# Optimization experiments

Measured on AMD Instinct MI355X. Metric: run time of the kernel, lower is better.

The kernel has to match this reference:

```python
import jax, jax.numpy as jnp
import numpy as np

DECAY = 0.8
COMMITMENT = 1.0
EPS = 1e-05


def setup_inputs() -> dict:
    key = jax.random.key(0)
    k1, k2 = jax.random.split(key)
    x = jax.random.normal(k1, (8, 4096, 256), dtype=jnp.float32)
    embed = jax.random.normal(k2, (8192, 256), dtype=jnp.float32)
    cluster_size = jnp.zeros((8192,), dtype=jnp.float32)
    embed_avg = embed  # torch registers embed_avg = embed.clone()
    return {"x": x, "embed": embed, "cluster_size": cluster_size, "embed_avg": embed_avg}


def reference(x, embed, cluster_size, embed_avg):
    # EuclideanCodebook.forward (training mode) + VectorQuantize straight-through.
    K, D = embed.shape
    shape = x.shape
    flatten = x.reshape(-1, D)  # [T, D], T = B*N

    dist = (2.0 * (flatten @ embed.T)
            - jnp.sum(flatten * flatten, axis=-1, keepdims=True)
            - jnp.sum(embed * embed, axis=-1)[None, :])  # [T, K]
    embed_ind = jnp.argmax(dist, axis=-1)  # [T]

    quantize = embed[embed_ind].reshape(shape)  # gather

    # EMA codebook statistics (scatter-add instead of materializing one-hot [T,K])
    bins = jax.ops.segment_sum(jnp.ones_like(embed_ind, dtype=x.dtype), embed_ind, num_segments=K)  # [K]
    embed_sum = jax.ops.segment_sum(flatten, embed_ind, num_segments=K)  # [K, D]

    new_cluster_size = cluster_size * DECAY + (1.0 - DECAY) * bins
    new_embed_avg = embed_avg * DECAY + (1.0 - DECAY) * embed_sum

    total = new_cluster_size.sum()
    smoothed = (new_cluster_size + EPS) / (total + K * EPS) * total  # laplace smoothing
    new_embed = new_embed_avg / smoothed[:, None]

    commit_loss = jnp.mean((jax.lax.stop_gradient(quantize) - x) ** 2) * COMMITMENT
    quantize_st = x + jax.lax.stop_gradient(quantize - x)  # straight-through

    ind_out = embed_ind.reshape(shape[:-1])
    return quantize_st, ind_out, commit_loss, new_embed, new_cluster_size, new_embed_avg
```

## Files before the change

kernel.cpp:

```cpp
#include <hip/hip_runtime.h>

#define DECAYF 0.8f
#define OMDF   0.2f
#define EPSF   1e-5f
#define COMMITF 1.0f
#define MARGINF 0.024f
#define FIXCAP  8192
#define MAXR    64

typedef _Float16 h8v __attribute__((ext_vector_type(8)));
typedef float f4v __attribute__((ext_vector_type(4)));

__device__ inline void gload_lds16(const void* g, void* l) {
  __builtin_amdgcn_global_load_lds(
      (const __attribute__((address_space(1))) unsigned int*)g,
      (__attribute__((address_space(3))) unsigned int*)l, 16, 0, 0);
}

__global__ __launch_bounds__(256) void k_pre(
    const float* __restrict__ embed, char* __restrict__ Ews,
    float* __restrict__ zero_p, int zero_n, float* __restrict__ ee, int K, int D)
{
  const int tid = threadIdx.x;
  const int gid0 = blockIdx.x * 256 + tid;
  const int gstride = gridDim.x * 256;

  for (int i = gid0; i < zero_n; i += gstride) zero_p[i] = 0.0f;

  for (int gid = gid0; gid < K * (D / 8); gid += gstride) {
    int k = gid >> 5;
    int d0 = (gid & 31) * 8;
    const float* ep = embed + (size_t)k * D + d0;
    float4 v0 = *(const float4*)(ep);
    float4 v1 = *(const float4*)(ep + 4);
    float f[8] = {v0.x, v0.y, v0.z, v0.w, v1.x, v1.y, v1.z, v1.w};
    h8v h;
    float ss = 0.f;
#pragma unroll
    for (int e = 0; e < 8; ++e) {
      h[e] = (_Float16)f[e];
      ss = fmaf(f[e], f[e], ss);
    }
    int tt = k >> 6;
    int c = k & 63;
    int byteoff = c * 512 + ((d0 * 2) ^ ((c & 7) << 4));
    *(h8v*)(Ews + (size_t)tt * 32768 + byteoff) = h;
#pragma unroll
    for (int off = 1; off < 32; off <<= 1) ss += __shfl_xor(ss, off);
    if ((gid & 31) == 0) ee[k] = 0.5f * ss;
  }
}

__device__ __forceinline__ void upd2(float s, int code, float& b1, float& b2, int& bi) {
  if (s > b1) { b2 = b1; b1 = s; bi = code; }
  else if (s > b2) { b2 = s; }
}

__device__ __forceinline__ void k_body(
    int TT, int NT, char* lds, const char* Ews, const float* ee,
    int w, int lane, int ch, int l15, int rowbyte0,
    const int (&dbyte)[8],
    const h8v (&xh)[2][8],
    f4v (&CUR)[2][2], f4v (&PRV)[2][2],
    float EEP0, float EEP1, float& EEC0, float& EEC1,
    float (&best)[2][4], float (&bst2)[2][4], int (&bidx)[2][4])
{
  const int k0 = TT * 64;
  const char* cb = lds + (TT & 1) * 32768;
  if (TT + 1 < NT) {
    const char* src = Ews + (size_t)(TT + 1) * 32768 + w * 8192 + lane * 16;
    char* dst = lds + ((TT + 1) & 1) * 32768 + w * 8192;
#pragma unroll
    for (int q = 0; q < 8; ++q) gload_lds16(src + q * 1024, dst + q * 1024);
  }
  EEC0 = ee[k0 + ch * 32 + l15];
  EEC1 = ee[k0 + ch * 32 + l15 + 16];
  const int c0p = k0 - 64 + ch * 32 + l15;
  const int c1p = c0p + 16;
#pragma unroll
  for (int rf = 0; rf < 2; ++rf) {
    CUR[rf][0] = (f4v){0.f, 0.f, 0.f, 0.f};
    CUR[rf][1] = (f4v){0.f, 0.f, 0.f, 0.f};
  }
  h8v Bh0[2], Bh1[2];
  {
    const char* p = cb + rowbyte0 + dbyte[0];
    Bh0[0] = *(const h8v*)(p);
    Bh1[0] = *(const h8v*)(p + 8192);
  }
#pragma unroll
  for (int ks = 0; ks < 8; ++ks) {
    const int cs = ks & 1, ns = cs ^ 1;
    if (ks < 7) {
      const char* p = cb + rowbyte0 + dbyte[ks + 1];
      Bh0[ns] = *(const h8v*)(p);
      Bh1[ns] = *(const h8v*)(p + 8192);
    }
    __builtin_amdgcn_s_setprio(1);
    CUR[0][0] = __builtin_amdgcn_mfma_f32_16x16x32_f16(xh[0][ks], Bh0[cs], CUR[0][0], 0, 0, 0);
    CUR[0][1] = __builtin_amdgcn_mfma_f32_16x16x32_f16(xh[0][ks], Bh1[cs], CUR[0][1], 0, 0, 0);
    CUR[1][0] = __builtin_amdgcn_mfma_f32_16x16x32_f16(xh[1][ks], Bh0[cs], CUR[1][0], 0, 0, 0);
    CUR[1][1] = __builtin_amdgcn_mfma_f32_16x16x32_f16(xh[1][ks], Bh1[cs], CUR[1][1], 0, 0, 0);
    __builtin_amdgcn_s_setprio(0);
    {
      const int rf = ks >> 2, ii = ks & 3;
      upd2(PRV[rf][0][ii] - EEP0, c0p, best[rf][ii], bst2[rf][ii], bidx[rf][ii]);
      upd2(PRV[rf][1][ii] - EEP1, c1p, best[rf][ii], bst2[rf][ii], bidx[rf][ii]);
    }
  }
  __syncthreads();
}

__global__ __launch_bounds__(256, 2) void k_dist(
    const float* __restrict__ x, const char* __restrict__ Ews,
    const float* __restrict__ ee, float* __restrict__ ind_f,
    int* __restrict__ idx_out, int* __restrict__ wl, int* __restrict__ cnt,
    int* __restrict__ cntr, int* __restrict__ rlist,
    int* __restrict__ olist, int* __restrict__ ocnt,
    int T, int K)
{
  extern __shared__ char lds[];
  const int tid = threadIdx.x;
  const int w = tid >> 6, lane = tid & 63;
  const int l15 = lane & 15, lk = lane >> 4;
  const int rgrp = w >> 1, ch = w & 1;
  const int row0 = blockIdx.x * 64 + rgrp * 32;
  const int NT = K / 64;

  h8v xh[2][8];
#pragma unroll
  for (int rf = 0; rf < 2; ++rf) {
    const float* xp = x + (size_t)(row0 + rf * 16 + l15) * 256 + lk * 8;
#pragma unroll
    for (int ks = 0; ks < 8; ++ks) {
      float4 v0 = *(const float4*)(xp + ks * 32);
      float4 v1 = *(const float4*)(xp + ks * 32 + 4);
      float f[8] = {v0.x, v0.y, v0.z, v0.w, v1.x, v1.y, v1.z, v1.w};
      h8v h;
#pragma unroll
      for (int e = 0; e < 8; ++e) h[e] = (_Float16)f[e];
      xh[rf][ks] = h;
    }
  }

  float best[2][4], bst2[2][4];
  int bidx[2][4];
#pragma unroll
  for (int rf = 0; rf < 2; ++rf)
#pragma unroll
    for (int i = 0; i < 4; ++i) { best[rf][i] = -3.0e38f; bst2[rf][i] = -3.0e38f; bidx[rf][i] = 0; }

  const int swz = (l15 & 7) << 4;
  const int rowbyte0 = (ch * 32 + l15) * 512;
  int dbyte[8];
#pragma unroll
  for (int ks = 0; ks < 8; ++ks) dbyte[ks] = (ks * 64 + lk * 16) ^ swz;

  {
    const char* src = Ews + (size_t)w * 8192 + lane * 16;
    char* dst = lds + w * 8192;
#pragma unroll
    for (int q = 0; q < 8; ++q)
      gload_lds16(src + q * 1024, dst + q * 1024);
  }
  __syncthreads();

  f4v accA[2][2], accB[2][2];
#pragma unroll
  for (int rf = 0; rf < 2; ++rf) {
    accB[rf][0] = (f4v){-3.0e38f, -3.0e38f, -3.0e38f, -3.0e38f};
    accB[rf][1] = (f4v){-3.0e38f, -3.0e38f, -3.0e38f, -3.0e38f};
  }
  float eeX0 = 0.f, eeX1 = 0.f, eeY0 = 0.f, eeY1 = 0.f;

  for (int tt = 0; tt < NT; tt += 2) {
    k_body(tt,     NT, lds, Ews, ee, w, lane, ch, l15, rowbyte0, dbyte, xh,
           accA, accB, eeX0, eeX1, eeY0, eeY1, best, bst2, bidx);
    k_body(tt + 1, NT, lds, Ews, ee, w, lane, ch, l15, rowbyte0, dbyte, xh,
           accB, accA, eeY0, eeY1, eeX0, eeX1, best, bst2, bidx);
  }
  {
    const int c0 = (NT - 1) * 64 + ch * 32 + l15, c1 = c0 + 16;
#pragma unroll
    for (int rf = 0; rf < 2; ++rf)
#pragma unroll
      for (int ii = 0; ii < 4; ++ii) {
        upd2(accB[rf][0][ii] - eeX0, c0, best[rf][ii], bst2[rf][ii], bidx[rf][ii]);
        upd2(accB[rf][1][ii] - eeX1, c1, best[rf][ii], bst2[rf][ii], bidx[rf][ii]);
      }
  }

#pragma unroll
  for (int rf = 0; rf < 2; ++rf)
#pragma unroll
    for (int i = 0; i < 4; ++i) {
      float s = best[rf][i], s2 = bst2[rf][i];
      int mi = bidx[rf][i];
#pragma unroll
      for (int off = 1; off < 16; off <<= 1) {
        float os = __shfl_xor(s, off);
        float os2 = __shfl_xor(s2, off);
        int oi = __shfl_xor(mi, off);
        if (os > s || (os == s && oi < mi)) {
          s2 = fmaxf(s, os2);
          s = os; mi = oi;
        } else {
          s2 = fmaxf(s2, os);
        }
      }
      best[rf][i] = s; bst2[rf][i] = s2; bidx[rf][i] = mi;
    }

  float* S  = (float*)lds;
  float* S2 = S + 128;
  int*   MI = (int*)(S2 + 128);
  if (l15 == 0) {
#pragma unroll
    for (int rf = 0; rf < 2; ++rf)
#pragma unroll
      for (int i = 0; i < 4; ++i) {
        int rl = rf * 16 + lk * 4 + i;
        int a = rgrp * 64 + ch * 32 + rl;
        S[a]  = best[rf][i];
        S2[a] = bst2[rf][i];
        MI[a] = bidx[rf][i];
      }
  }
  __syncthreads();
  if (ch == 0 && lane < 32) {
    int a0 = rgrp * 64 + lane;
    float sA = S[a0],      s2A = S2[a0];      int miA = MI[a0];
    float sB = S[a0 + 32], s2B = S2[a0 + 32]; int miB = MI[a0 + 32];
    float s, s2; int mi;
    if (sB > sA || (sB == sA && miB < miA)) { s = sB; mi = miB; s2 = fmaxf(sA, s2B); }
    else                                    { s = sA; mi = miA; s2 = fmaxf(s2A, sB); }
    int row = row0 + lane;
    idx_out[row] = mi;
    ind_f[row] = (float)mi;
    int flagged = 0;
    if (s - s2 < MARGINF) {
      int slot = atomicAdd(cnt, 1);
      if (slot < FIXCAP) { wl[slot] = row; flagged = 1; }
    }
    if (!flagged) {
      int slot2 = atomicAdd(&cntr[mi], 1);
      if (slot2 < MAXR) rlist[mi * MAXR + slot2] = row;
      else { int o = atomicAdd(ocnt, 1); olist[o] = row; }
    }
  }
}

__global__ __launch_bounds__(256) void k_fix1(
    const float* __restrict__ x, const float* __restrict__ embed,
    const float* __restrict__ ee, const int* __restrict__ wl,
    const int* __restrict__ cnt, float* __restrict__ pval,
    int* __restrict__ pidx)
{
  __shared__ float Xs[8][256];
  const int b = blockIdx.x & 255;
  const int g = blockIdx.x >> 8;
  const int t = threadIdx.x;
  int n = *cnt; if (n > FIXCAP) n = FIXCAP;
  const int c = b * 32 + (t & 31);
  const float* er = embed + (size_t)c * 256;
  const float eec = ee[c];
  const int rl = t >> 5;

  for (int r0 = g * 8; r0 < n; r0 += 32) {
    __syncthreads();
    for (int i = t; i < 8 * 64; i += 256) {
      int rr = i >> 6, dq = i & 63;
      int wi = r0 + rr; if (wi >= n) wi = n - 1;
      int row = wl[wi];
      ((float4*)Xs[rr])[dq] = *(const float4*)(x + (size_t)row * 256 + dq * 4);
    }
    __syncthreads();
    const float* xr = Xs[rl];
    float s0 = 0.f, s1 = 0.f, s2a = 0.f, s3 = 0.f;
#pragma unroll
    for (int d = 0; d < 256; d += 16) {
      float4 e0 = *(const float4*)(er + d);
      float4 e1 = *(const float4*)(er + d + 4);
      float4 e2 = *(const float4*)(er + d + 8);
      float4 e3 = *(const float4*)(er + d + 12);
      s0 = fmaf(xr[d + 0], e0.x, s0);  s0 = fmaf(xr[d + 1], e0.y, s0);
      s0 = fmaf(xr[d + 2], e0.z, s0);  s0 = fmaf(xr[d + 3], e0.w, s0);
      s1 = fmaf(xr[d + 4], e1.x, s1);  s1 = fmaf(xr[d + 5], e1.y, s1);
      s1 = fmaf(xr[d + 6], e1.z, s1);  s1 = fmaf(xr[d + 7], e1.w, s1);
      s2a = fmaf(xr[d + 8], e2.x, s2a);  s2a = fmaf(xr[d + 9], e2.y, s2a);
      s2a = fmaf(xr[d + 10], e2.z, s2a); s2a = fmaf(xr[d + 11], e2.w, s2a);
      s3 = fmaf(xr[d + 12], e3.x, s3);  s3 = fmaf(xr[d + 13], e3.y, s3);
      s3 = fmaf(xr[d + 14], e3.z, s3);  s3 = fmaf(xr[d + 15], e3.w, s3);
    }
    float s = ((s0 + s1) + (s2a + s3)) - eec;
    int mi = c;
#pragma unroll
    for (int off = 1; off < 32; off <<= 1) {
      float os = __shfl_xor(s, off);
      int oi = __shfl_xor(mi, off);
      if (os > s || (os == s && oi < mi)) { s = os; mi = oi; }
    }
    int wi = r0 + rl;
    if ((t & 31) == 0 && wi < n) {
      pval[(size_t)wi * 256 + b] = s;
      pidx[(size_t)wi * 256 + b] = mi;
    }
  }
}

__global__ __launch_bounds__(256) void k_fix2(
    const int* __restrict__ wl, const int* __restrict__ cnt,
    const float* __restrict__ pval, const int* __restrict__ pidx,
    float* __restrict__ ind_f, int* __restrict__ idx_out,
    int* __restrict__ cntr, int* __restrict__ rlist,
    int* __restrict__ olist, int* __restrict__ ocnt)
{
  __shared__ float bv[256];
  __shared__ int bi[256];
  const int t = threadIdx.x;
  int n = *cnt; if (n > FIXCAP) n = FIXCAP;
  for (int it = blockIdx.x; it < n; it += gridDim.x) {
    __syncthreads();
    bv[t] = pval[(size_t)it * 256 + t];
    bi[t] = pidx[(size_t)it * 256 + t];
    __syncthreads();
    for (int sh = 128; sh > 0; sh >>= 1) {
      if (t < sh) {
        if (bv[t + sh] > bv[t] || (bv[t + sh] == bv[t] && bi[t + sh] < bi[t])) {
          bv[t] = bv[t + sh]; bi[t] = bi[t + sh];
        }
      }
      __syncthreads();
    }
    if (t == 0) {
      int row = wl[it];
      int kf = bi[0];
      idx_out[row] = kf;
      ind_f[row] = (float)kf;
      int slot = atomicAdd(&cntr[kf], 1);
      if (slot < MAXR) rlist[kf * MAXR + slot] = row;
      else { int o = atomicAdd(ocnt, 1); olist[o] = row; }
    }
  }
}

__global__ void k_gather(const float* __restrict__ x, const float* __restrict__ embed,
                         const int* __restrict__ idx, float* __restrict__ quant,
                         float* __restrict__ lslots, int T, int D)
{
  int wave = threadIdx.x >> 6;
  int lane = threadIdx.x & 63;
  int row = blockIdx.x * 4 + wave;
  if (row >= T) return;
  int k = idx[row];
  const float* xr = x + (size_t)row * D;
  const float* er = embed + (size_t)k * D;
  float* qr = quant + (size_t)row * D;
  float lsum = 0.f;
  for (int d = lane * 4; d < D; d += 256) {
    float4 xv = *reinterpret_cast<const float4*>(xr + d);
    float4 ev = *reinterpret_cast<const float4*>(er + d);
    *reinterpret_cast<float4*>(qr + d) = ev;
    float dx = ev.x - xv.x, dy = ev.y - xv.y, dz = ev.z - xv.z, dw = ev.w - xv.w;
    lsum += dx * dx + dy * dy + dz * dz + dw * dw;
  }
  for (int off = 32; off > 0; off >>= 1) lsum += __shfl_down(lsum, off);
  if (lane == 0) atomicAdd(&lslots[row & 255], lsum);
}

__global__ __launch_bounds__(256) void k_mid(
    const float* __restrict__ cs, const int* __restrict__ cntr,
    float* __restrict__ ncs, float* __restrict__ total_acc,
    const float* __restrict__ lslots, float* __restrict__ out_loss, float scale,
    const float* __restrict__ x, const int* __restrict__ idx,
    const int* __restrict__ olist, const int* __restrict__ ocnt,
    float* __restrict__ ovfsum, int K)
{
  const int tid = threadIdx.x;
  const int wave = tid >> 6, lane = tid & 63;
  if (blockIdx.x == 32) {
    float v = lslots[tid];
    for (int off = 32; off > 0; off >>= 1) v += __shfl_down(v, off);
    __shared__ float s4[4];
    if ((tid & 63) == 0) s4[tid >> 6] = v;
    __syncthreads();
    if (tid == 0) out_loss[0] = (s4[0] + s4[1] + s4[2] + s4[3]) * scale;
    return;
  }
  int k = blockIdx.x * 256 + tid;
  float v = cs[k] * DECAYF + OMDF * (float)cntr[k];
  ncs[k] = v;
  for (int off = 32; off > 0; off >>= 1) v += __shfl_down(v, off);
  __shared__ float s4[4];
  if ((tid & 63) == 0) s4[tid >> 6] = v;
  __syncthreads();
  if (tid == 0) atomicAdd(total_acc, s4[0] + s4[1] + s4[2] + s4[3]);
  int n = *ocnt;
  for (int i = blockIdx.x * 4 + wave; i < n; i += 128) {
    int row = olist[i];
    int kk = idx[row];
    int d0 = lane * 4;
    float4 xv = *(const float4*)(x + (size_t)row * 256 + d0);
    atomicAdd(&ovfsum[(size_t)kk * 256 + d0 + 0], xv.x);
    atomicAdd(&ovfsum[(size_t)kk * 256 + d0 + 1], xv.y);
    atomicAdd(&ovfsum[(size_t)kk * 256 + d0 + 2], xv.z);
    atomicAdd(&ovfsum[(size_t)kk * 256 + d0 + 3], xv.w);
  }
}

__global__ __launch_bounds__(256) void k_ema2(
    const float* __restrict__ x, const float* __restrict__ ea,
    const int* __restrict__ cntr, const int* __restrict__ rlist,
    const float* __restrict__ ovfsum, const float* __restrict__ ncs,
    const float* __restrict__ total_acc, float* __restrict__ ne,
    float* __restrict__ nea, int K, int D)
{
  int wave = threadIdx.x >> 6, lane = threadIdx.x & 63;
  int k = blockIdx.x * 4 + wave;
  if (k >= K) return;
  int c = cntr[k];
  int m = c < MAXR ? c : MAXR;
  int d0 = lane * 4;
  float4 s = *(const float4*)(ovfsum + (size_t)k * 256 + d0);
  for (int i = 0; i < m; ++i) {
    int r = rlist[k * MAXR + i];
    float4 xv = *(const float4*)(x + (size_t)r * 256 + d0);
    s.x += xv.x; s.y += xv.y; s.z += xv.z; s.w += xv.w;
  }
  float4 eav = *(const float4*)(ea + (size_t)k * 256 + d0);
  float total = *total_acc;
  float csk = ncs[k];
  float sm = (csk + EPSF) / (total + (float)K * EPSF) * total;
  float rs = 1.0f / sm;
  float v0 = eav.x * DECAYF + OMDF * s.x;
  float v1 = eav.y * DECAYF + OMDF * s.y;
  float v2 = eav.z * DECAYF + OMDF * s.z;
  float v3 = eav.w * DECAYF + OMDF * s.w;
  size_t o = (size_t)k * 256 + d0;
  nea[o + 0] = v0; nea[o + 1] = v1; nea[o + 2] = v2; nea[o + 3] = v3;
  ne[o + 0] = v0 * rs; ne[o + 1] = v1 * rs; ne[o + 2] = v2 * rs; ne[o + 3] = v3 * rs;
}

extern "C" void kernel_launch(void* const* d_in, const int* in_sizes, int n_in,
                              void* d_out, int out_size, void* d_ws, size_t ws_size,
                              hipStream_t stream)
{
  const float* x     = (const float*)d_in[0];
  const float* embed = (const float*)d_in[1];
  const float* cs    = (const float*)d_in[2];
  const float* ea    = (const float*)d_in[3];
  const int K = in_sizes[2];
  const int D = in_sizes[1] / K;
  const int T = in_sizes[0] / D;

  float* out   = (float*)d_out;
  float* o_q   = out;
  float* o_ind = out + (size_t)T * D;
  float* o_ls  = o_ind + T;
  float* o_ne  = o_ls + 1;
  float* o_ncs = o_ne + (size_t)K * D;
  float* o_nea = o_ncs + K;

  float* w      = (float*)d_ws;
  float* ee     = w;
  int*   idx    = (int*)(w + K);
  int*   wl     = idx + T;
  float* pval   = (float*)(wl + FIXCAP);
  int*   pidx   = (int*)(pval + (size_t)FIXCAP * 256);
  int*   rlist  = pidx + (size_t)FIXCAP * 256;
  int*   olist  = rlist + (size_t)K * MAXR;
  float* ovfsum = (float*)(olist + T);
  float* lslots = ovfsum + (size_t)K * D;
  float* total  = lslots + 256;
  int*   cnt    = (int*)(total + 1);
  int*   cntr   = cnt + 1;
  int*   ocnt   = cntr + K;
  int zero_n = K * D + 256 + 1 + 1 + K + 1;
  size_t ews_off = (((size_t)(ocnt + 1 - (int*)w)) + 63) & ~(size_t)63;
  char* Ews = (char*)(w + ews_off);

  k_pre<<<2048, 256, 0, stream>>>(embed, Ews, ovfsum, zero_n, ee, K, D);
  k_dist<<<T / 64, 256, 65536, stream>>>(x, Ews, ee, o_ind, idx, wl, cnt,
                                         cntr, rlist, olist, ocnt, T, K);
  k_fix1<<<1024, 256, 0, stream>>>(x, embed, ee, wl, cnt, pval, pidx);
  k_fix2<<<1024, 256, 0, stream>>>(wl, cnt, pval, pidx, o_ind, idx,
                                   cntr, rlist, olist, ocnt);
  k_gather<<<(T + 3) / 4, 256, 0, stream>>>(x, embed, idx, o_q, lslots, T, D);
  k_mid<<<33, 256, 0, stream>>>(cs, cntr, o_ncs, total, lslots, o_ls,
                                COMMITF / ((float)T * (float)D),
                                x, idx, olist, ocnt, ovfsum, K);
  k_ema2<<<(K + 3) / 4, 256, 0, stream>>>(x, ea, cntr, rlist, ovfsum, o_ncs, total,
                                          o_ne, o_nea, K, D);
}
```

Baseline: 462.3 us.

## Fuse quantize gather and commit loss into per-code EMA and overflow passes

Drops the standalone gather kernel. Each row's quantized output and loss term are now produced while that row is visited in the per-codeword EMA accumulation (rlist) or in the overflow pass in k_mid. This avoids a second full read of x and the per-row embed gather, and each codeword's embed row is read once per wave. A small final kernel reduces the loss slots. The cost is that quant writes become scattered by codeword order instead of sequential, and load balance now depends on cluster sizes.

```diff
diff --git a/kernel.cpp b/kernel.cpp
--- a/kernel.cpp
+++ b/kernel.cpp
@@ -344,49 +344,16 @@
   }
 }
 
-__global__ void k_gather(const float* __restrict__ x, const float* __restrict__ embed,
-                         const int* __restrict__ idx, float* __restrict__ quant,
-                         float* __restrict__ lslots, int T, int D)
-{
-  int wave = threadIdx.x >> 6;
-  int lane = threadIdx.x & 63;
-  int row = blockIdx.x * 4 + wave;
-  if (row >= T) return;
-  int k = idx[row];
-  const float* xr = x + (size_t)row * D;
-  const float* er = embed + (size_t)k * D;
-  float* qr = quant + (size_t)row * D;
-  float lsum = 0.f;
-  for (int d = lane * 4; d < D; d += 256) {
-    float4 xv = *reinterpret_cast<const float4*>(xr + d);
-    float4 ev = *reinterpret_cast<const float4*>(er + d);
-    *reinterpret_cast<float4*>(qr + d) = ev;
-    float dx = ev.x - xv.x, dy = ev.y - xv.y, dz = ev.z - xv.z, dw = ev.w - xv.w;
-    lsum += dx * dx + dy * dy + dz * dz + dw * dw;
-  }
-  for (int off = 32; off > 0; off >>= 1) lsum += __shfl_down(lsum, off);
-  if (lane == 0) atomicAdd(&lslots[row & 255], lsum);
-}
-
 __global__ __launch_bounds__(256) void k_mid(
     const float* __restrict__ cs, const int* __restrict__ cntr,
     float* __restrict__ ncs, float* __restrict__ total_acc,
-    const float* __restrict__ lslots, float* __restrict__ out_loss, float scale,
-    const float* __restrict__ x, const int* __restrict__ idx,
-    const int* __restrict__ olist, const int* __restrict__ ocnt,
-    float* __restrict__ ovfsum, int K)
+    const float* __restrict__ x, const float* __restrict__ embed,
+    const int* __restrict__ idx, const int* __restrict__ olist,
+    const int* __restrict__ ocnt, float* __restrict__ ovfsum,
+    float* __restrict__ quant, float* __restrict__ lslots, int K)
 {
   const int tid = threadIdx.x;
   const int wave = tid >> 6, lane = tid & 63;
-  if (blockIdx.x == 32) {
-    float v = lslots[tid];
-    for (int off = 32; off > 0; off >>= 1) v += __shfl_down(v, off);
-    __shared__ float s4[4];
-    if ((tid & 63) == 0) s4[tid >> 6] = v;
-    __syncthreads();
-    if (tid == 0) out_loss[0] = (s4[0] + s4[1] + s4[2] + s4[3]) * scale;
-    return;
-  }
   int k = blockIdx.x * 256 + tid;
   float v = cs[k] * DECAYF + OMDF * (float)cntr[k];
   ncs[k] = v;
@@ -401,19 +368,27 @@
     int kk = idx[row];
     int d0 = lane * 4;
     float4 xv = *(const float4*)(x + (size_t)row * 256 + d0);
+    float4 ev = *(const float4*)(embed + (size_t)kk * 256 + d0);
     atomicAdd(&ovfsum[(size_t)kk * 256 + d0 + 0], xv.x);
     atomicAdd(&ovfsum[(size_t)kk * 256 + d0 + 1], xv.y);
     atomicAdd(&ovfsum[(size_t)kk * 256 + d0 + 2], xv.z);
     atomicAdd(&ovfsum[(size_t)kk * 256 + d0 + 3], xv.w);
+    *(float4*)(quant + (size_t)row * 256 + d0) = ev;
+    float dx = ev.x - xv.x, dy = ev.y - xv.y, dz = ev.z - xv.z, dw = ev.w - xv.w;
+    float l = dx * dx + dy * dy + dz * dz + dw * dw;
+    for (int off = 32; off > 0; off >>= 1) l += __shfl_down(l, off);
+    if (lane == 0) atomicAdd(&lslots[row & 255], l);
   }
 }
 
 __global__ __launch_bounds__(256) void k_ema2(
     const float* __restrict__ x, const float* __restrict__ ea,
+    const float* __restrict__ embed,
     const int* __restrict__ cntr, const int* __restrict__ rlist,
     const float* __restrict__ ovfsum, const float* __restrict__ ncs,
     const float* __restrict__ total_acc, float* __restrict__ ne,
-    float* __restrict__ nea, int K, int D)
+    float* __restrict__ nea, float* __restrict__ quant,
+    float* __restrict__ lslots, int K, int D)
 {
   int wave = threadIdx.x >> 6, lane = threadIdx.x & 63;
   int k = blockIdx.x * 4 + wave;
@@ -421,11 +396,16 @@
   int c = cntr[k];
   int m = c < MAXR ? c : MAXR;
   int d0 = lane * 4;
+  float4 ev = *(const float4*)(embed + (size_t)k * 256 + d0);
   float4 s = *(const float4*)(ovfsum + (size_t)k * 256 + d0);
+  float lsum = 0.f;
   for (int i = 0; i < m; ++i) {
     int r = rlist[k * MAXR + i];
     float4 xv = *(const float4*)(x + (size_t)r * 256 + d0);
     s.x += xv.x; s.y += xv.y; s.z += xv.z; s.w += xv.w;
+    *(float4*)(quant + (size_t)r * 256 + d0) = ev;
+    float dx = ev.x - xv.x, dy = ev.y - xv.y, dz = ev.z - xv.z, dw = ev.w - xv.w;
+    lsum += dx * dx + dy * dy + dz * dz + dw * dw;
   }
   float4 eav = *(const float4*)(ea + (size_t)k * 256 + d0);
   float total = *total_acc;
@@ -439,6 +419,20 @@
   size_t o = (size_t)k * 256 + d0;
   nea[o + 0] = v0; nea[o + 1] = v1; nea[o + 2] = v2; nea[o + 3] = v3;
   ne[o + 0] = v0 * rs; ne[o + 1] = v1 * rs; ne[o + 2] = v2 * rs; ne[o + 3] = v3 * rs;
+  for (int off = 32; off > 0; off >>= 1) lsum += __shfl_down(lsum, off);
+  if (lane == 0 && m > 0) atomicAdd(&lslots[k & 255], lsum);
+}
+
+__global__ void k_loss(const float* __restrict__ lslots, float* __restrict__ out_loss,
+                       float scale)
+{
+  int tid = threadIdx.x;
+  float v = lslots[tid];
+  for (int off = 32; off > 0; off >>= 1) v += __shfl_down(v, off);
+  __shared__ float s4[4];
+  if ((tid & 63) == 0) s4[tid >> 6] = v;
+  __syncthreads();
+  if (tid == 0) out_loss[0] = (s4[0] + s4[1] + s4[2] + s4[3]) * scale;
 }
 
 extern "C" void kernel_launch(void* const* d_in, const int* in_sizes, int n_in,
@@ -485,10 +479,9 @@
   k_fix1<<<1024, 256, 0, stream>>>(x, embed, ee, wl, cnt, pval, pidx);
   k_fix2<<<1024, 256, 0, stream>>>(wl, cnt, pval, pidx, o_ind, idx,
                                    cntr, rlist, olist, ocnt);
-  k_gather<<<(T + 3) / 4, 256, 0, stream>>>(x, embed, idx, o_q, lslots, T, D);
-  k_mid<<<33, 256, 0, stream>>>(cs, cntr, o_ncs, total, lslots, o_ls,
-                                COMMITF / ((float)T * (float)D),
-                                x, idx, olist, ocnt, ovfsum, K);
-  k_ema2<<<(K + 3) / 4, 256, 0, stream>>>(x, ea, cntr, rlist, ovfsum, o_ncs, total,
-                                          o_ne, o_nea, K, D);
-}
+  k_mid<<<32, 256, 0, stream>>>(cs, cntr, o_ncs, total, x, embed, idx,
+                                olist, ocnt, ovfsum, o_q, lslots, K);
+  k_ema2<<<(K + 3) / 4, 256, 0, stream>>>(x, ea, embed, cntr, rlist, ovfsum,
+                                          o_ncs, total, o_ne, o_nea, o_q, lslots, K, D);
+  k_loss<<<1, 256, 0, stream>>>(lslots, o_ls, COMMITF / ((float)T * (float)D));
+}
```

Measured after the change: 421.2 us (median of 2 runs). -8.9%, faster.
